# Kernel optimization log

Hardware: AMD Instinct MI355X
Metric: run time of the kernel (lower is better)

Reference implementation:

```python
import jax, jax.numpy as jnp
import numpy as np

EMBED = 2048
HEADS = 16


def setup_inputs() -> dict:
    key = jax.random.key(0)
    ks = jax.random.split(key, 9)
    N, L, E = 4, 2048, EMBED
    inp = {
        "query": jax.random.normal(ks[0], (N, L, E), dtype=jnp.float32),
        "keys": jax.random.normal(ks[1], (N, L, E), dtype=jnp.float32),
        "values": jax.random.normal(ks[2], (N, L, E), dtype=jnp.float32),
        "mask": jax.random.randint(ks[3], (N, L), 0, 2, dtype=jnp.int32),
        # nn.Linear weights, stored torch-style as (out_features, in_features)
        "Wq": jax.random.normal(ks[4], (E, E), dtype=jnp.float32) * (E ** -0.5),
        "Wk": jax.random.normal(ks[5], (E, E), dtype=jnp.float32) * (E ** -0.5),
        "Wv": jax.random.normal(ks[6], (E, E), dtype=jnp.float32) * (E ** -0.5),
        "Wo": jax.random.normal(ks[7], (E, E), dtype=jnp.float32) * (E ** -0.5),
        "bo": jax.random.normal(ks[8], (E,), dtype=jnp.float32) * 0.01,
    }
    return inp


def reference(query, keys, values, mask, Wq, Wk, Wv, Wo, bo):
    N, Lq, E = query.shape
    Lk = keys.shape[1]
    H = HEADS
    D = E // H
    # projections (torch Linear: y = x @ W.T)
    q = (query @ Wq.T).reshape(N, Lq, H, D)   # nqhd
    k = (keys @ Wk.T).reshape(N, Lk, H, D)    # nkhd
    v = (values @ Wv.T).reshape(N, Lk, H, D)  # nkhd
    # attention scores per head: (N, H, Lq, Lk)
    energy = jnp.einsum('nqhd,nkhd->nhqk', q, k)
    # 2D mask (N, Lk): 0 = masked out, broadcast over heads and query positions
    m = mask[:, None, None, :]
    energy = jnp.where(m == 0, jnp.float32(-1e20), energy)
    # source scales by sqrt(embed_size), not sqrt(head_dim)
    attn = jax.nn.softmax(energy * (E ** -0.5), axis=-1)
    out = jnp.einsum('nhqk,nkhd->nqhd', attn, v).reshape(N, Lq, E)
    return out @ Wo.T + bo
```

## Files before the change

### kernel.cpp

```cpp
#include <hip/hip_runtime.h>
#include <stdint.h>


typedef __bf16 bf16;
typedef __bf16 bf16x4 __attribute__((ext_vector_type(4)));
typedef __bf16 bf16x8 __attribute__((ext_vector_type(8)));
typedef float  f32x4  __attribute__((ext_vector_type(4)));

#define MFMA16(a, b, c) __builtin_amdgcn_mfma_f32_16x16x32_bf16(a, b, c, 0, 0, 0)

__device__ __forceinline__ void gload_lds16(const void* g, void* s) {
  __builtin_amdgcn_global_load_lds(
      (const __attribute__((address_space(1))) void*)g,
      (__attribute__((address_space(3))) void*)s, 16, 0, 0);
}

__global__ __launch_bounds__(256) void cvt_bf16(const float* __restrict__ src,
                                                bf16* __restrict__ dst, long n) {
  long i = ((long)blockIdx.x * 256 + threadIdx.x) * 4;
  if (i < n) {
    f32x4 f = *(const f32x4*)(src + i);
    bf16x4 h = { (bf16)f.x, (bf16)f.y, (bf16)f.z, (bf16)f.w };
    *(bf16x4*)(dst + i) = h;
  }
}

__global__ __launch_bounds__(256) void gather_cvt(const float* __restrict__ src,
                                                  bf16* __restrict__ dst,
                                                  const int* __restrict__ idx) {
  long i = (long)blockIdx.x * 256 + threadIdx.x;
  int row = (int)(i >> 8);
  int u = (int)(i & 255);
  int n = row >> 11, p = row & 2047;
  long srow = ((long)n << 11) + idx[(n << 11) + p];
  const float* s = src + srow * 2048 + u * 8;
  f32x4 a = *(const f32x4*)s;
  f32x4 b = *(const f32x4*)(s + 4);
  bf16x8 h = { (bf16)a.x, (bf16)a.y, (bf16)a.z, (bf16)a.w,
               (bf16)b.x, (bf16)b.y, (bf16)b.z, (bf16)b.w };
  *(bf16x8*)(dst + (long)row * 2048 + u * 8) = h;
}

__global__ __launch_bounds__(256) void mask_compact(const int* __restrict__ mask,
                                                    int* __restrict__ idx,
                                                    int* __restrict__ cnts) {
  const int n = blockIdx.x;
  const int t = threadIdx.x, l = t & 63, w = t >> 6;
  const int* m = mask + n * 2048;
  __shared__ int wtot[4];
  int f[8], tt = 0;
  const int base = t * 8;
#pragma unroll
  for (int i = 0; i < 8; ++i) { f[i] = (m[base + i] != 0); tt += f[i]; }
  int sc = tt;
#pragma unroll
  for (int d = 1; d < 64; d <<= 1) {
    int v = __shfl_up(sc, d);
    if (l >= d) sc += v;
  }
  if (l == 63) wtot[w] = sc;
  __syncthreads();
  int woff = 0;
#pragma unroll
  for (int i = 0; i < 4; ++i) if (i < w) woff += wtot[i];
  int off = woff + sc - tt;
#pragma unroll
  for (int i = 0; i < 8; ++i)
    if (f[i]) { idx[n * 2048 + off] = base + i; ++off; }
  int total = wtot[0] + wtot[1] + wtot[2] + wtot[3];
  for (int p = total + t; p < 2048; p += 256) idx[n * 2048 + p] = 2047;
  if (t == 0) { cnts[n] = total; cnts[4 + n] = (total + 127) & ~127; }
}

template <int AEXIT, int OUT_F32, int ADD_BIAS>
__global__ __launch_bounds__(512, 2) void gemm256(const bf16* __restrict__ A,
                                                  const bf16* __restrict__ B,
                                                  void* __restrict__ Cout,
                                                  const float* __restrict__ bias,
                                                  const int* __restrict__ cnts) {
  constexpr int K = 2048, LDC = 2048, NT = 32;
  constexpr int TILE = 256 * 64;
  __shared__ bf16 S[2 * 2 * TILE];
  const int t = threadIdx.x;
  const int l = t & 63, w = t >> 6;
  const int wr = w >> 2, wc = w & 3;
  const int l15 = l & 15, l4 = l >> 4;

  const int Mb = ((blockIdx.x & 7) << 2) + (blockIdx.x >> 3);
  const long tm = (long)Mb * 256;
  const long tn = (long)blockIdx.y * 256;

  if constexpr (AEXIT) {
    int n = (int)(tm >> 11);
    if ((int)(tm & 2047) >= cnts[4 + n]) return;
  }

  const bf16* Ab = A + tm * K;
  const bf16* Bb = B + tn * K;

  auto stage = [&](int T, int p) {
    bf16* sA = S + p * 2 * TILE;
    bf16* sB = sA + TILE;
    const bf16* Ak = Ab + T * 64;
    const bf16* Bk = Bb + T * 64;
#pragma unroll
    for (int i = 0; i < 4; ++i) {
      int u = i * 512 + t;
      int row = u >> 3, slot = u & 7;
      int ss = slot ^ (row & 7);
      gload_lds16(Ak + (long)row * K + ss * 8, sA + u * 8);
    }
#pragma unroll
    for (int i = 0; i < 4; ++i) {
      int u = i * 512 + t;
      int row = u >> 3, slot = u & 7;
      int ss = slot ^ (row & 7);
      gload_lds16(Bk + (long)row * K + ss * 8, sB + u * 8);
    }
  };

  f32x4 acc[8][4];
#pragma unroll
  for (int i = 0; i < 8; ++i)
#pragma unroll
    for (int j = 0; j < 4; ++j) acc[i][j] = (f32x4){0.f, 0.f, 0.f, 0.f};

  stage(0, 0);

  for (int T = 0; T < NT; ++T) {
    const int p = T & 1;
    const bf16* sA = S + p * 2 * TILE;
    const bf16* sB = sA + TILE;

    asm volatile("" ::: "memory");
    __builtin_amdgcn_s_barrier();
    asm volatile("" ::: "memory");
    if (T + 1 < NT) {
      stage(T + 1, p ^ 1);
      asm volatile("s_waitcnt vmcnt(8)" ::: "memory");
    } else {
      asm volatile("s_waitcnt vmcnt(0)" ::: "memory");
    }
    __builtin_amdgcn_s_barrier();
    asm volatile("" ::: "memory");

#pragma unroll
    for (int kk = 0; kk < 2; ++kk) {
      bf16x8 af[8], bf[4];
#pragma unroll
      for (int mi = 0; mi < 8; ++mi) {
        int row = wr * 128 + mi * 16 + l15;
        int slot = (kk * 4 + l4) ^ (row & 7);
        af[mi] = *(const bf16x8*)(sA + row * 64 + slot * 8);
      }
#pragma unroll
      for (int ni = 0; ni < 4; ++ni) {
        int row = wc * 64 + ni * 16 + l15;
        int slot = (kk * 4 + l4) ^ (row & 7);
        bf[ni] = *(const bf16x8*)(sB + row * 64 + slot * 8);
      }
      __builtin_amdgcn_s_setprio(1);
#pragma unroll
      for (int mi = 0; mi < 8; ++mi)
#pragma unroll
        for (int ni = 0; ni < 4; ++ni)
          acc[mi][ni] = MFMA16(af[mi], bf[ni], acc[mi][ni]);
      __builtin_amdgcn_s_setprio(0);
    }
  }

#pragma unroll
  for (int mi = 0; mi < 8; ++mi) {
#pragma unroll
    for (int ni = 0; ni < 4; ++ni) {
      long col = tn + wc * 64 + ni * 16 + l15;
      long row = tm + wr * 128 + mi * 16 + l4 * 4;
#pragma unroll
      for (int r = 0; r < 4; ++r) {
        float v = acc[mi][ni][r];
        if constexpr (OUT_F32) {
          if constexpr (ADD_BIAS) v += bias[col];
          ((float*)Cout)[(row + r) * (long)LDC + col] = v;
        } else {
          ((bf16*)Cout)[(row + r) * (long)LDC + col] = (bf16)v;
        }
      }
    }
  }
}

__global__ __launch_bounds__(256) void attn_fwd(const bf16* __restrict__ Qp,
                                                const bf16* __restrict__ Kp,
                                                const bf16* __restrict__ Vp,
                                                const int* __restrict__ cnts,
                                                bf16* __restrict__ Op) {
  constexpr int L = 2048, E = 2048, D = 128, KVB = 64;
  __shared__ bf16 Kt[KVB * D];
  __shared__ bf16 VT[D * KVB];
  __shared__ bf16 Pt[128 * 72];
  const int t = threadIdx.x, l = t & 63, w = t >> 6;
  const int l15 = l & 15, l4 = l >> 4;
  const int n = blockIdx.y >> 4, h = blockIdx.y & 15;
  const int q0 = blockIdx.x * 128;
  const int wq = w * 32;
  const float scale = 0.022097086912079608f;

  const bf16* Qb = Qp + ((long)n * L + q0) * E + h * D;
  const bf16* Kb = Kp + (long)n * L * E + h * D;
  const bf16* Vb = Vp + (long)n * L * E + h * D;
  const int cnt = cnts[n];
  const int ntk = (cnt + 63) >> 6;

  bf16x8 qf[2][4];
#pragma unroll
  for (int mi = 0; mi < 2; ++mi)
#pragma unroll
    for (int kk = 0; kk < 4; ++kk)
      qf[mi][kk] = *(const bf16x8*)(Qb + (long)(wq + mi * 16 + l15) * E + kk * 32 + l4 * 8);

  f32x4 o[2][8];
#pragma unroll
  for (int mi = 0; mi < 2; ++mi)
#pragma unroll
    for (int ni = 0; ni < 8; ++ni) o[mi][ni] = (f32x4){0.f, 0.f, 0.f, 0.f};
  float mreg[2] = {-1e20f, -1e20f};
  float lreg[2] = {0.f, 0.f};

  const int vd0 = (t >> 4) * 8;
  const int vj0 = (t & 15) * 4;

  for (int ti = 0; ti < ntk; ++ti) {
    const int kv = ti << 6;
#pragma unroll
    for (int i = 0; i < 4; ++i) {
      int chunk = w * 4 + i;
      int row = chunk * 4 + l4;
      int srcslot = l15 ^ (row & 7);
      gload_lds16(Kb + (long)(kv + row) * E + srcslot * 8, Kt + chunk * 512);
    }
    bf16x8 vr[4];
#pragma unroll
    for (int r = 0; r < 4; ++r)
      vr[r] = *(const bf16x8*)(Vb + (long)(kv + vj0 + r) * E + vd0);
#pragma unroll
    for (int i = 0; i < 8; ++i) {
      int d = vd0 + i;
      bf16x4 pk = { vr[0][i], vr[1][i], vr[2][i], vr[3][i] };
      *(bf16x4*)(VT + d * KVB + (vj0 ^ ((d & 7) << 3))) = pk;
    }
    __syncthreads();

    f32x4 s[2][4];
#pragma unroll
    for (int mi = 0; mi < 2; ++mi)
#pragma unroll
      for (int ni = 0; ni < 4; ++ni) s[mi][ni] = (f32x4){0.f, 0.f, 0.f, 0.f};
#pragma unroll
    for (int kk = 0; kk < 4; ++kk) {
      bf16x8 kf[4];
#pragma unroll
      for (int ni = 0; ni < 4; ++ni) {
        int row = ni * 16 + l15;
        int slot = (kk * 4 + l4) ^ (l15 & 7);
        kf[ni] = *(const bf16x8*)(Kt + row * D + slot * 8);
      }
#pragma unroll
      for (int mi = 0; mi < 2; ++mi)
#pragma unroll
        for (int ni = 0; ni < 4; ++ni)
          s[mi][ni] = MFMA16(kf[ni], qf[mi][kk], s[mi][ni]);
    }

    if (kv + KVB > cnt) {
#pragma unroll
      for (int mi = 0; mi < 2; ++mi)
#pragma unroll
        for (int ni = 0; ni < 4; ++ni)
#pragma unroll
          for (int r = 0; r < 4; ++r) {
            int j = kv + ni * 16 + l4 * 4 + r;
            s[mi][ni][r] = (j < cnt) ? s[mi][ni][r] * scale : -1e20f;
          }
    } else {
#pragma unroll
      for (int mi = 0; mi < 2; ++mi)
#pragma unroll
        for (int ni = 0; ni < 4; ++ni)
#pragma unroll
          for (int r = 0; r < 4; ++r) s[mi][ni][r] *= scale;
    }

    bool need[2];
    float corr[2];
#pragma unroll
    for (int mi = 0; mi < 2; ++mi) {
      float vmax = -1e20f;
#pragma unroll
      for (int ni = 0; ni < 4; ++ni)
#pragma unroll
        for (int r = 0; r < 4; ++r) vmax = fmaxf(vmax, s[mi][ni][r]);
      vmax = fmaxf(vmax, __shfl_xor(vmax, 16));
      vmax = fmaxf(vmax, __shfl_xor(vmax, 32));
      bool nd = vmax > mreg[mi] + 8.0f;
      float mn = nd ? vmax : mreg[mi];
      corr[mi] = nd ? __expf(mreg[mi] - vmax) : 1.0f;
      need[mi] = nd;
      mreg[mi] = mn;
      float rsum = 0.f;
#pragma unroll
      for (int ni = 0; ni < 4; ++ni) {
        bf16x4 pk;
#pragma unroll
        for (int r = 0; r < 4; ++r) {
          float p = __expf(s[mi][ni][r] - mn);
          rsum += p;
          pk[r] = (bf16)p;
        }
        *(bf16x4*)(Pt + (wq + mi * 16 + l15) * 72 + ni * 16 + l4 * 4) = pk;
      }
      rsum += __shfl_xor(rsum, 16);
      rsum += __shfl_xor(rsum, 32);
      lreg[mi] = lreg[mi] * corr[mi] + rsum;
    }
    if (__any(need[0] || need[1])) {
#pragma unroll
      for (int mi = 0; mi < 2; ++mi) {
#pragma unroll
        for (int r = 0; r < 4; ++r) {
          float cr = __shfl(corr[mi], (l >> 4) * 20 + r);
#pragma unroll
          for (int ni = 0; ni < 8; ++ni) o[mi][ni][r] *= cr;
        }
      }
    }

#pragma unroll
    for (int kk = 0; kk < 2; ++kk) {
      bf16x8 pa[2], vb[8];
#pragma unroll
      for (int mi = 0; mi < 2; ++mi)
        pa[mi] = *(const bf16x8*)(Pt + (wq + mi * 16 + l15) * 72 + kk * 32 + l4 * 8);
#pragma unroll
      for (int ni = 0; ni < 8; ++ni) {
        int d = ni * 16 + l15;
        int col = (kk * 32 + l4 * 8) ^ ((d & 7) << 3);
        vb[ni] = *(const bf16x8*)(VT + d * KVB + col);
      }
#pragma unroll
      for (int mi = 0; mi < 2; ++mi)
#pragma unroll
        for (int ni = 0; ni < 8; ++ni)
          o[mi][ni] = MFMA16(pa[mi], vb[ni], o[mi][ni]);
    }
    __syncthreads();
  }

  float inv[2];
#pragma unroll
  for (int mi = 0; mi < 2; ++mi) inv[mi] = 1.f / lreg[mi];
#pragma unroll
  for (int mi = 0; mi < 2; ++mi) {
#pragma unroll
    for (int r = 0; r < 4; ++r) {
      float iv = __shfl(inv[mi], (l >> 4) * 20 + r);
      long grow = (long)n * L + q0 + wq + mi * 16 + l4 * 4 + r;
#pragma unroll
      for (int ni = 0; ni < 8; ++ni)
        Op[grow * E + h * D + ni * 16 + l15] = (bf16)(o[mi][ni][r] * iv);
    }
  }
}

extern "C" void kernel_launch(void* const* d_in, const int* in_sizes, int n_in,
                              void* d_out, int out_size, void* d_ws, size_t ws_size,
                              hipStream_t stream) {
  (void)in_sizes; (void)n_in; (void)out_size; (void)ws_size;
  const float* query = (const float*)d_in[0];
  const float* keys  = (const float*)d_in[1];
  const float* values= (const float*)d_in[2];
  const int*   mask  = (const int*)d_in[3];
  const float* Wq = (const float*)d_in[4];
  const float* Wk = (const float*)d_in[5];
  const float* Wv = (const float*)d_in[6];
  const float* Wo = (const float*)d_in[7];
  const float* bo = (const float*)d_in[8];
  float* out = (float*)d_out;

  const int N = 4, L = 2048, E = 2048;
  const int M = N * L;
  const long EE = (long)E * E;
  const long ME = (long)M * E;

  int*  idx  = (int*)d_ws;
  int*  cnts = idx + N * 2048;
  bf16* wslot= (bf16*)((char*)d_ws + 65536);
  bf16* xs   = wslot + EE;
  bf16* qp   = xs + ME;
  bf16* kp   = qp + ME;
  bf16* vp   = kp + ME;

  const int cbw = (int)(EE / 4 / 256);
  const int cba = (int)(ME / 4 / 256);
  const int gbl = (int)(ME / 8 / 256);
  dim3 gg(32, 8);

  mask_compact<<<4, 256, 0, stream>>>(mask, idx, cnts);

  cvt_bf16<<<cbw, 256, 0, stream>>>(Wq, wslot, EE);
  cvt_bf16<<<cba, 256, 0, stream>>>(query, xs, ME);
  gemm256<0, 0, 0><<<gg, 512, 0, stream>>>(xs, wslot, qp, nullptr, cnts);

  cvt_bf16<<<cbw, 256, 0, stream>>>(Wk, wslot, EE);
  gather_cvt<<<gbl, 256, 0, stream>>>(keys, xs, idx);
  gemm256<1, 0, 0><<<gg, 512, 0, stream>>>(xs, wslot, kp, nullptr, cnts);

  cvt_bf16<<<cbw, 256, 0, stream>>>(Wv, wslot, EE);
  gather_cvt<<<gbl, 256, 0, stream>>>(values, xs, idx);
  gemm256<1, 0, 0><<<gg, 512, 0, stream>>>(xs, wslot, vp, nullptr, cnts);

  attn_fwd<<<dim3(L / 128, N * 16), 256, 0, stream>>>(qp, kp, vp, cnts, qp);

  cvt_bf16<<<cbw, 256, 0, stream>>>(Wo, wslot, EE);
  gemm256<0, 1, 1><<<gg, 512, 0, stream>>>(qp, wslot, out, bo, cnts);
}
```

Measured before the change: 496.2 us.

## Double-buffer K/V tiles and pass P through registers in attention kernel

Rewrites the attention kernel to run 512 threads per block, each wave handling 16 query rows instead of 32. K and V tiles are double-buffered in LDS so the next tile loads while the current one computes. The softmax probabilities move into MFMA operand layout through cross-lane shuffles instead of an LDS P buffer, and blocks are remapped through a 1D grid with swizzled ordering. This aims to hide global-load latency and raise occupancy, at the cost of more LDS per block and extra shuffle instructions.

```diff
diff --git a/kernel.cpp b/kernel.cpp
--- a/kernel.cpp
+++ b/kernel.cpp
@@ -3,9 +3,11 @@
 
 
 typedef __bf16 bf16;
+typedef __bf16 bf16x2 __attribute__((ext_vector_type(2)));
 typedef __bf16 bf16x4 __attribute__((ext_vector_type(4)));
 typedef __bf16 bf16x8 __attribute__((ext_vector_type(8)));
 typedef float  f32x4  __attribute__((ext_vector_type(4)));
+typedef uint32_t u32x4 __attribute__((ext_vector_type(4)));
 
 #define MFMA16(a, b, c) __builtin_amdgcn_mfma_f32_16x16x32_bf16(a, b, c, 0, 0, 0)
 
@@ -13,6 +15,10 @@
   __builtin_amdgcn_global_load_lds(
       (const __attribute__((address_space(1))) void*)g,
       (__attribute__((address_space(3))) void*)s, 16, 0, 0);
+}
+
+__device__ __forceinline__ uint32_t pkbf(float a, float b) {
+  return __builtin_bit_cast(uint32_t, (bf16x2){(bf16)a, (bf16)b});
 }
 
 __global__ __launch_bounds__(256) void cvt_bf16(const float* __restrict__ src,
@@ -189,185 +195,188 @@
   }
 }
 
-__global__ __launch_bounds__(256) void attn_fwd(const bf16* __restrict__ Qp,
-                                                const bf16* __restrict__ Kp,
-                                                const bf16* __restrict__ Vp,
-                                                const int* __restrict__ cnts,
-                                                bf16* __restrict__ Op) {
-  constexpr int L = 2048, E = 2048, D = 128, KVB = 64;
-  __shared__ bf16 Kt[KVB * D];
-  __shared__ bf16 VT[D * KVB];
-  __shared__ bf16 Pt[128 * 72];
+__global__ __launch_bounds__(512, 4) void attn_fwd(const bf16* __restrict__ Qp,
+                                                   const bf16* __restrict__ Kp,
+                                                   const bf16* __restrict__ Vp,
+                                                   const int* __restrict__ cnts,
+                                                   bf16* __restrict__ Op) {
+  constexpr int L = 2048, E = 2048, KVB = 64;
+  __shared__ bf16 Kt[2][KVB * 128];
+  __shared__ bf16 VT[2][128 * KVB];
   const int t = threadIdx.x, l = t & 63, w = t >> 6;
   const int l15 = l & 15, l4 = l >> 4;
-  const int n = blockIdx.y >> 4, h = blockIdx.y & 15;
-  const int q0 = blockIdx.x * 128;
-  const int wq = w * 32;
+
+  const int b = blockIdx.x;
+  const int slot = ((b & 7) << 7) + (b >> 3);
+  const int q0 = (slot & 15) << 7;
+  const int y = slot >> 4;
+  const int n = y >> 4, h = y & 15;
+  const int wq = w * 16;
   const float scale = 0.022097086912079608f;
 
-  const bf16* Qb = Qp + ((long)n * L + q0) * E + h * D;
-  const bf16* Kb = Kp + (long)n * L * E + h * D;
-  const bf16* Vb = Vp + (long)n * L * E + h * D;
+  const bf16* Qb = Qp + ((long)n * L + q0) * E + h * 128;
+  const bf16* Kb = Kp + (long)n * L * E + h * 128;
+  const bf16* Vb = Vp + (long)n * L * E + h * 128;
   const int cnt = cnts[n];
   const int ntk = (cnt + 63) >> 6;
 
-  bf16x8 qf[2][4];
-#pragma unroll
-  for (int mi = 0; mi < 2; ++mi)
-#pragma unroll
-    for (int kk = 0; kk < 4; ++kk)
-      qf[mi][kk] = *(const bf16x8*)(Qb + (long)(wq + mi * 16 + l15) * E + kk * 32 + l4 * 8);
-
-  f32x4 o[2][8];
-#pragma unroll
-  for (int mi = 0; mi < 2; ++mi)
-#pragma unroll
-    for (int ni = 0; ni < 8; ++ni) o[mi][ni] = (f32x4){0.f, 0.f, 0.f, 0.f};
-  float mreg[2] = {-1e20f, -1e20f};
-  float lreg[2] = {0.f, 0.f};
-
-  const int vd0 = (t >> 4) * 8;
-  const int vj0 = (t & 15) * 4;
-
-  for (int ti = 0; ti < ntk; ++ti) {
-    const int kv = ti << 6;
+  bf16x8 qf[4];
+#pragma unroll
+  for (int kk = 0; kk < 4; ++kk)
+    qf[kk] = *(const bf16x8*)(Qb + (long)(wq + l15) * E + kk * 32 + l4 * 8);
+
+  f32x4 o[8];
+#pragma unroll
+  for (int ni = 0; ni < 8; ++ni) o[ni] = (f32x4){0.f, 0.f, 0.f, 0.f};
+  float mreg = -1e20f, lreg = 0.f;
+
+  const int vd0 = (t & 31) * 4;
+  const int vj0 = (t >> 5) * 4;
+
+  auto stageK = [&](int kv, int pp) {
+#pragma unroll
+    for (int i = 0; i < 2; ++i) {
+      int u = i * 512 + t;
+      int row = u >> 4, sl = u & 15;
+      gload_lds16(Kb + (long)(kv + row) * E + ((sl ^ (row & 7)) * 8),
+                  &Kt[pp][u * 8]);
+    }
+  };
+  auto loadV = [&](int kv, bf16x4* vr) {
+#pragma unroll
+    for (int r = 0; r < 4; ++r)
+      vr[r] = *(const bf16x4*)(Vb + (long)(kv + vj0 + r) * E + vd0);
+  };
+  auto writeV = [&](const bf16x4* vr, int pp) {
 #pragma unroll
     for (int i = 0; i < 4; ++i) {
-      int chunk = w * 4 + i;
-      int row = chunk * 4 + l4;
-      int srcslot = l15 ^ (row & 7);
-      gload_lds16(Kb + (long)(kv + row) * E + srcslot * 8, Kt + chunk * 512);
-    }
-    bf16x8 vr[4];
-#pragma unroll
-    for (int r = 0; r < 4; ++r)
-      vr[r] = *(const bf16x8*)(Vb + (long)(kv + vj0 + r) * E + vd0);
-#pragma unroll
-    for (int i = 0; i < 8; ++i) {
       int d = vd0 + i;
       bf16x4 pk = { vr[0][i], vr[1][i], vr[2][i], vr[3][i] };
-      *(bf16x4*)(VT + d * KVB + (vj0 ^ ((d & 7) << 3))) = pk;
-    }
-    __syncthreads();
-
-    f32x4 s[2][4];
-#pragma unroll
-    for (int mi = 0; mi < 2; ++mi)
-#pragma unroll
-      for (int ni = 0; ni < 4; ++ni) s[mi][ni] = (f32x4){0.f, 0.f, 0.f, 0.f};
+      *(bf16x4*)(&VT[pp][d * KVB + (vj0 ^ ((d & 7) << 3))]) = pk;
+    }
+  };
+
+  bf16x4 vr[4];
+  stageK(0, 0);
+  loadV(0, vr);
+  writeV(vr, 0);
+  __syncthreads();
+
+  for (int ti = 0; ti < ntk; ++ti) {
+    const int p = ti & 1;
+    const int kv = ti << 6;
+    const bool pre = (ti + 1) < ntk;
+    if (pre) {
+      stageK(kv + KVB, p ^ 1);
+      loadV(kv + KVB, vr);
+    }
+
+    f32x4 s[4];
+#pragma unroll
+    for (int ni = 0; ni < 4; ++ni) s[ni] = (f32x4){0.f, 0.f, 0.f, 0.f};
 #pragma unroll
     for (int kk = 0; kk < 4; ++kk) {
       bf16x8 kf[4];
 #pragma unroll
       for (int ni = 0; ni < 4; ++ni) {
         int row = ni * 16 + l15;
-        int slot = (kk * 4 + l4) ^ (l15 & 7);
-        kf[ni] = *(const bf16x8*)(Kt + row * D + slot * 8);
-      }
-#pragma unroll
-      for (int mi = 0; mi < 2; ++mi)
-#pragma unroll
-        for (int ni = 0; ni < 4; ++ni)
-          s[mi][ni] = MFMA16(kf[ni], qf[mi][kk], s[mi][ni]);
+        int sl = (kk * 4 + l4) ^ (row & 7);
+        kf[ni] = *(const bf16x8*)(&Kt[p][row * 128 + sl * 8]);
+      }
+#pragma unroll
+      for (int ni = 0; ni < 4; ++ni)
+        s[ni] = MFMA16(kf[ni], qf[kk], s[ni]);
     }
 
     if (kv + KVB > cnt) {
 #pragma unroll
-      for (int mi = 0; mi < 2; ++mi)
-#pragma unroll
-        for (int ni = 0; ni < 4; ++ni)
-#pragma unroll
-          for (int r = 0; r < 4; ++r) {
-            int j = kv + ni * 16 + l4 * 4 + r;
-            s[mi][ni][r] = (j < cnt) ? s[mi][ni][r] * scale : -1e20f;
-          }
+      for (int ni = 0; ni < 4; ++ni)
+#pragma unroll
+        for (int r = 0; r < 4; ++r) {
+          int j = kv + ni * 16 + l4 * 4 + r;
+          s[ni][r] = (j < cnt) ? s[ni][r] * scale : -1e20f;
+        }
     } else {
 #pragma unroll
-      for (int mi = 0; mi < 2; ++mi)
-#pragma unroll
-        for (int ni = 0; ni < 4; ++ni)
-#pragma unroll
-          for (int r = 0; r < 4; ++r) s[mi][ni][r] *= scale;
-    }
-
-    bool need[2];
-    float corr[2];
-#pragma unroll
-    for (int mi = 0; mi < 2; ++mi) {
-      float vmax = -1e20f;
-#pragma unroll
       for (int ni = 0; ni < 4; ++ni)
 #pragma unroll
-        for (int r = 0; r < 4; ++r) vmax = fmaxf(vmax, s[mi][ni][r]);
-      vmax = fmaxf(vmax, __shfl_xor(vmax, 16));
-      vmax = fmaxf(vmax, __shfl_xor(vmax, 32));
-      bool nd = vmax > mreg[mi] + 8.0f;
-      float mn = nd ? vmax : mreg[mi];
-      corr[mi] = nd ? __expf(mreg[mi] - vmax) : 1.0f;
-      need[mi] = nd;
-      mreg[mi] = mn;
-      float rsum = 0.f;
-#pragma unroll
-      for (int ni = 0; ni < 4; ++ni) {
-        bf16x4 pk;
-#pragma unroll
-        for (int r = 0; r < 4; ++r) {
-          float p = __expf(s[mi][ni][r] - mn);
-          rsum += p;
-          pk[r] = (bf16)p;
-        }
-        *(bf16x4*)(Pt + (wq + mi * 16 + l15) * 72 + ni * 16 + l4 * 4) = pk;
-      }
-      rsum += __shfl_xor(rsum, 16);
-      rsum += __shfl_xor(rsum, 32);
-      lreg[mi] = lreg[mi] * corr[mi] + rsum;
-    }
-    if (__any(need[0] || need[1])) {
-#pragma unroll
-      for (int mi = 0; mi < 2; ++mi) {
-#pragma unroll
-        for (int r = 0; r < 4; ++r) {
-          float cr = __shfl(corr[mi], (l >> 4) * 20 + r);
-#pragma unroll
-          for (int ni = 0; ni < 8; ++ni) o[mi][ni][r] *= cr;
-        }
-      }
-    }
-
+        for (int r = 0; r < 4; ++r) s[ni][r] *= scale;
+    }
+
+    float vmax = -1e20f;
+#pragma unroll
+    for (int ni = 0; ni < 4; ++ni)
+#pragma unroll
+      for (int r = 0; r < 4; ++r) vmax = fmaxf(vmax, s[ni][r]);
+    vmax = fmaxf(vmax, __shfl_xor(vmax, 16));
+    vmax = fmaxf(vmax, __shfl_xor(vmax, 32));
+    bool nd = vmax > mreg + 8.0f;
+    float corr = nd ? __expf(mreg - vmax) : 1.0f;
+    float mn = nd ? vmax : mreg;
+    mreg = mn;
+    float rsum = 0.f;
+    uint32_t u[4][2];
+#pragma unroll
+    for (int ni = 0; ni < 4; ++ni) {
+      float p0 = __expf(s[ni][0] - mn);
+      float p1 = __expf(s[ni][1] - mn);
+      float p2 = __expf(s[ni][2] - mn);
+      float p3 = __expf(s[ni][3] - mn);
+      rsum += (p0 + p1) + (p2 + p3);
+      u[ni][0] = pkbf(p0, p1);
+      u[ni][1] = pkbf(p2, p3);
+    }
+    rsum += __shfl_xor(rsum, 16);
+    rsum += __shfl_xor(rsum, 32);
+    lreg = lreg * corr + rsum;
+    if (__any(nd)) {
+#pragma unroll
+      for (int r = 0; r < 4; ++r) {
+        float cr = __shfl(corr, l4 * 20 + r);
+#pragma unroll
+        for (int ni = 0; ni < 8; ++ni) o[ni][r] *= cr;
+      }
+    }
+
+    const int srcA = l15 + ((l & 16) << 1);
+    const int srcB = srcA + 16;
+    const bool e5 = (l4 >> 1) != 0;
 #pragma unroll
     for (int kk = 0; kk < 2; ++kk) {
-      bf16x8 pa[2], vb[8];
-#pragma unroll
-      for (int mi = 0; mi < 2; ++mi)
-        pa[mi] = *(const bf16x8*)(Pt + (wq + mi * 16 + l15) * 72 + kk * 32 + l4 * 8);
+      uint32_t a0 = (uint32_t)__shfl((int)u[kk * 2][0], srcA);
+      uint32_t a1 = (uint32_t)__shfl((int)u[kk * 2][1], srcA);
+      uint32_t a2 = (uint32_t)__shfl((int)u[kk * 2][0], srcB);
+      uint32_t a3 = (uint32_t)__shfl((int)u[kk * 2][1], srcB);
+      uint32_t b0 = (uint32_t)__shfl((int)u[kk * 2 + 1][0], srcA);
+      uint32_t b1 = (uint32_t)__shfl((int)u[kk * 2 + 1][1], srcA);
+      uint32_t b2 = (uint32_t)__shfl((int)u[kk * 2 + 1][0], srcB);
+      uint32_t b3 = (uint32_t)__shfl((int)u[kk * 2 + 1][1], srcB);
+      u32x4 pw = { e5 ? b0 : a0, e5 ? b1 : a1, e5 ? b2 : a2, e5 ? b3 : a3 };
+      bf16x8 pa = __builtin_bit_cast(bf16x8, pw);
+      bf16x8 vb[8];
 #pragma unroll
       for (int ni = 0; ni < 8; ++ni) {
         int d = ni * 16 + l15;
         int col = (kk * 32 + l4 * 8) ^ ((d & 7) << 3);
-        vb[ni] = *(const bf16x8*)(VT + d * KVB + col);
-      }
-#pragma unroll
-      for (int mi = 0; mi < 2; ++mi)
-#pragma unroll
-        for (int ni = 0; ni < 8; ++ni)
-          o[mi][ni] = MFMA16(pa[mi], vb[ni], o[mi][ni]);
-    }
+        vb[ni] = *(const bf16x8*)(&VT[p][d * KVB + col]);
+      }
+#pragma unroll
+      for (int ni = 0; ni < 8; ++ni)
+        o[ni] = MFMA16(pa, vb[ni], o[ni]);
+    }
+
+    if (pre) writeV(vr, p ^ 1);
     __syncthreads();
   }
 
-  float inv[2];
-#pragma unroll
-  for (int mi = 0; mi < 2; ++mi) inv[mi] = 1.f / lreg[mi];
-#pragma unroll
-  for (int mi = 0; mi < 2; ++mi) {
-#pragma unroll
-    for (int r = 0; r < 4; ++r) {
-      float iv = __shfl(inv[mi], (l >> 4) * 20 + r);
-      long grow = (long)n * L + q0 + wq + mi * 16 + l4 * 4 + r;
-#pragma unroll
-      for (int ni = 0; ni < 8; ++ni)
-        Op[grow * E + h * D + ni * 16 + l15] = (bf16)(o[mi][ni][r] * iv);
-    }
+  float inv = 1.f / lreg;
+#pragma unroll
+  for (int r = 0; r < 4; ++r) {
+    float iv = __shfl(inv, l4 * 20 + r);
+    long grow = (long)n * L + q0 + wq + l4 * 4 + r;
+#pragma unroll
+    for (int ni = 0; ni < 8; ++ni)
+      Op[grow * E + h * 128 + ni * 16 + l15] = (bf16)(o[ni][r] * iv);
   }
 }
 
@@ -418,7 +427,7 @@
   gather_cvt<<<gbl, 256, 0, stream>>>(values, xs, idx);
   gemm256<1, 0, 0><<<gg, 512, 0, stream>>>(xs, wslot, vp, nullptr, cnts);
 
-  attn_fwd<<<dim3(L / 128, N * 16), 256, 0, stream>>>(qp, kp, vp, cnts, qp);
+  attn_fwd<<<1024, 512, 0, stream>>>(qp, kp, vp, cnts, qp);
 
   cvt_bf16<<<cbw, 256, 0, stream>>>(Wo, wslot, EE);
   gemm256<0, 1, 1><<<gg, 512, 0, stream>>>(qp, wslot, out, bo, cnts);
```

New measurement: 478.7 us. 1.04x faster.
